# Performance work log

Measured on AMD Instinct MI355X. Metric: run time of the kernel, lower is better.

The kernel has to match this reference:

```python
import jax, jax.numpy as jnp
from jax import lax
import numpy as np

DECAY = 0.9
THRESH = 1.0


def setup_inputs() -> dict:
    key = jax.random.key(0)
    k1, k2, k3 = jax.random.split(key, 3)
    B, T, I, H, O = 64, 256, 1024, 2048, 1024
    x = jax.random.normal(k1, (B, T, I), dtype=jnp.float32)
    W1 = jax.random.normal(k2, (I, H), dtype=jnp.float32) * (1.0 / np.sqrt(I))
    b1 = jnp.zeros((H,), dtype=jnp.float32)
    W2 = jax.random.normal(k3, (H, O), dtype=jnp.float32) * (1.0 / np.sqrt(H))
    b2 = jnp.zeros((O,), dtype=jnp.float32)
    return {"x": x, "W1": W1, "b1": b1, "W2": W2, "b2": b2}


def reference(x, W1, b1, W2, b2):
    B, T, I = x.shape
    H = W1.shape[1]
    # Batch fc1 across all timesteps in one GEMM: [B,T,H]
    cur = jnp.einsum('bti,ih->bth', x, W1) + b1
    cur_tm = jnp.swapaxes(cur, 0, 1)  # [T,B,H] time-major for scan

    def step(carry, cur_t):
        mem, _ = carry
        mem = mem * DECAY + cur_t * (1.0 - DECAY)
        fired = mem > THRESH
        spk = jnp.where(fired, 1.0, 0.0).astype(mem.dtype)
        mem = jnp.where(fired, 0.0, mem)
        return (mem, spk), None

    mem0 = jnp.zeros((B, H), dtype=x.dtype)
    spk0 = jnp.zeros((B, H), dtype=x.dtype)
    (_, spk_last), _ = lax.scan(step, (mem0, spk0), cur_tm)
    # fc2 applied only to the final spike pattern, as in the original
    return spk_last @ W2 + b2
```

## Files before the change

### kernel.cpp

```cpp
#include <hip/hip_runtime.h>


typedef __attribute__((ext_vector_type(4))) float f32x4;
typedef __attribute__((ext_vector_type(8))) short s16x8;

#define GPTR(p) ((const __attribute__((address_space(1))) void*)(p))
#define SPTR(p) ((__attribute__((address_space(3))) void*)(p))

static constexpr int Bsz = 64, Tsz = 256, Isz = 1024, Hsz = 2048, Osz = 1024;
static constexpr int KB = 32;
static constexpr int NB = 64;

__device__ __forceinline__ unsigned short f2bf(float f) {
  unsigned u = __float_as_uint(f);
  u += 0x7FFFu + ((u >> 16) & 1u);
  return (unsigned short)(u >> 16);
}
__device__ __forceinline__ float bf2f(unsigned short h) {
  return __uint_as_float(((unsigned)h) << 16);
}

__global__ void split_x_kernel(const float* __restrict__ x,
                               unsigned short* __restrict__ hi,
                               unsigned short* __restrict__ lo) {
  const long i = (long)blockIdx.x * 256 + threadIdx.x;
  const float4 v = ((const float4*)x)[i];
  const unsigned short hx = f2bf(v.x), hy = f2bf(v.y), hz = f2bf(v.z), hw = f2bf(v.w);
  ushort4 H, L;
  H.x = hx; H.y = hy; H.z = hz; H.w = hw;
  L.x = f2bf(v.x - bf2f(hx));
  L.y = f2bf(v.y - bf2f(hy));
  L.z = f2bf(v.z - bf2f(hz));
  L.w = f2bf(v.w - bf2f(hw));
  ((ushort4*)hi)[i] = H;
  ((ushort4*)lo)[i] = L;
}

__global__ void w1_transpose_split_kernel(const float* __restrict__ W1,
                                          unsigned short* __restrict__ wh,
                                          unsigned short* __restrict__ wl) {
  __shared__ float tile[32][33];
  const int h0 = blockIdx.x * 32;
  const int i0 = blockIdx.y * 32;
  const int c = threadIdx.x & 31;
  const int r4 = threadIdx.x >> 5;
#pragma unroll
  for (int s = 0; s < 4; ++s) {
    const int r = r4 + s * 8;
    tile[r][c] = W1[(long)(i0 + r) * Hsz + h0 + c];
  }
  __syncthreads();
#pragma unroll
  for (int s = 0; s < 4; ++s) {
    const int hr = r4 + s * 8;
    const float v = tile[c][hr];
    const unsigned short hh = f2bf(v);
    wh[(long)(h0 + hr) * Isz + i0 + c] = hh;
    wl[(long)(h0 + hr) * Isz + i0 + c] = f2bf(v - bf2f(hh));
  }
}

__global__ __launch_bounds__(256, 3) void gemm1_scan_kernel(
    const unsigned short* __restrict__ xh, const unsigned short* __restrict__ xl,
    const unsigned short* __restrict__ wth, const unsigned short* __restrict__ wtl,
    const float* __restrict__ b1, float* __restrict__ spk) {
  __shared__ __align__(16) unsigned short lds[2 * Tsz * KB + 2 * NB * KB];
  unsigned short* ldsAh = lds;
  unsigned short* ldsAl = lds + Tsz * KB;
  unsigned short* ldsBh = lds + 2 * Tsz * KB;
  unsigned short* ldsBl = lds + 2 * Tsz * KB + NB * KB;

  const int tid = threadIdx.x;
  const int w = tid >> 6;
  const int l = tid & 63;
  const int b = blockIdx.y;
  const int hblk = blockIdx.x * NB;

  const int lr = l >> 2;
  const int lc = (l & 3) * 8;

  f32x4 acc[4][4];
#pragma unroll
  for (int i = 0; i < 4; ++i)
#pragma unroll
    for (int j = 0; j < 4; ++j)
      acc[i][j] = f32x4{0.f, 0.f, 0.f, 0.f};

  const long rowA0 = (long)b * Tsz;

  for (int kb = 0; kb < Isz / KB; ++kb) {
    const int k0 = kb * KB;
#pragma unroll
    for (int c = 0; c < 4; ++c) {
      const int rloc = w * 64 + c * 16;
      const unsigned short* gh = xh + (rowA0 + rloc + lr) * Isz + k0 + lc;
      const unsigned short* gl = xl + (rowA0 + rloc + lr) * Isz + k0 + lc;
      __builtin_amdgcn_global_load_lds(GPTR(gh), SPTR(ldsAh + rloc * KB), 16, 0, 0);
      __builtin_amdgcn_global_load_lds(GPTR(gl), SPTR(ldsAl + rloc * KB), 16, 0, 0);
    }
    {
      const int hloc = w * 16;
      const unsigned short* gh = wth + (long)(hblk + hloc + lr) * Isz + k0 + lc;
      const unsigned short* gl = wtl + (long)(hblk + hloc + lr) * Isz + k0 + lc;
      __builtin_amdgcn_global_load_lds(GPTR(gh), SPTR(ldsBh + hloc * KB), 16, 0, 0);
      __builtin_amdgcn_global_load_lds(GPTR(gl), SPTR(ldsBl + hloc * KB), 16, 0, 0);
    }
    __syncthreads();

    s16x8 ah[4], al[4];
    const int arow = w * 64 + (l & 15);
    const int koff = (l >> 4) * 8;
#pragma unroll
    for (int mi = 0; mi < 4; ++mi) {
      const int off = (arow + mi * 16) * KB + koff;
      ah[mi] = *(const s16x8*)(ldsAh + off);
      al[mi] = *(const s16x8*)(ldsAl + off);
    }
#pragma unroll
    for (int ni = 0; ni < 4; ++ni) {
      const int boff = (ni * 16 + (l & 15)) * KB + koff;
      const s16x8 bh = *(const s16x8*)(ldsBh + boff);
      const s16x8 bl = *(const s16x8*)(ldsBl + boff);
#pragma unroll
      for (int mi = 0; mi < 4; ++mi) {
        acc[mi][ni] = __builtin_amdgcn_mfma_f32_16x16x32_bf16(ah[mi], bh, acc[mi][ni], 0, 0, 0);
        acc[mi][ni] = __builtin_amdgcn_mfma_f32_16x16x32_bf16(ah[mi], bl, acc[mi][ni], 0, 0, 0);
        acc[mi][ni] = __builtin_amdgcn_mfma_f32_16x16x32_bf16(al[mi], bh, acc[mi][ni], 0, 0, 0);
      }
    }
    __syncthreads();
  }

  float* scanbuf = (float*)lds;
  float memv = 0.f;
  int fired = 0;
  const float b1v = (tid < NB) ? b1[hblk + tid] : 0.f;

  for (int p = 0; p < 4; ++p) {
    if (w == p) {
#pragma unroll
      for (int mi = 0; mi < 4; ++mi)
#pragma unroll
        for (int ni = 0; ni < 4; ++ni) {
          const int col = ni * 16 + (l & 15);
          const int trow = mi * 16 + (l >> 4) * 4;
#pragma unroll
          for (int r = 0; r < 4; ++r)
            scanbuf[(trow + r) * NB + col] = acc[mi][ni][r];
        }
    }
    __syncthreads();
    if (tid < NB) {
      for (int t = 0; t < 64; ++t) {
        const float c = scanbuf[t * NB + tid] + b1v;
        memv = memv * 0.9f + c * 0.1f;
        fired = memv > 1.0f;
        if (fired) memv = 0.f;
      }
    }
    __syncthreads();
  }
  if (tid < NB) spk[(long)b * Hsz + hblk + tid] = fired ? 1.0f : 0.0f;
}

__global__ void gemm2_kernel(const float* __restrict__ spk, const float* __restrict__ W2,
                             const float* __restrict__ b2, float* __restrict__ out) {
  __shared__ int s_cnt[256];
  __shared__ int s_off[257];
  __shared__ int s_list[Hsz];
  const int b = blockIdx.x;
  const int tid = threadIdx.x;
  int hs[8];
  int c = 0;
#pragma unroll
  for (int e = 0; e < 8; ++e) {
    const int h = tid * 8 + e;
    if (spk[(long)b * Hsz + h] > 0.5f) hs[c++] = h;
  }
  s_cnt[tid] = c;
  __syncthreads();
  if (tid == 0) {
    int s = 0;
    for (int i = 0; i < 256; ++i) { s_off[i] = s; s += s_cnt[i]; }
    s_off[256] = s;
  }
  __syncthreads();
  {
    const int base = s_off[tid];
    for (int i = 0; i < c; ++i) s_list[base + i] = hs[i];
  }
  __syncthreads();
  const int total = s_off[256];
#pragma unroll
  for (int q = 0; q < 4; ++q) {
    const int o = q * 256 + tid;
    float v = b2[o];
    for (int i = 0; i < total; ++i) v += W2[(long)s_list[i] * Osz + o];
    out[(long)b * Osz + o] = v;
  }
}

extern "C" void kernel_launch(void* const* d_in, const int* in_sizes, int n_in,
                              void* d_out, int out_size, void* d_ws, size_t ws_size,
                              hipStream_t stream) {
  const float* x  = (const float*)d_in[0];
  const float* W1 = (const float*)d_in[1];
  const float* b1 = (const float*)d_in[2];
  const float* W2 = (const float*)d_in[3];
  const float* b2 = (const float*)d_in[4];
  float* out = (float*)d_out;

  unsigned short* xh = (unsigned short*)d_ws;
  unsigned short* xl = xh + (long)Bsz * Tsz * Isz;
  unsigned short* wh = xl + (long)Bsz * Tsz * Isz;
  unsigned short* wl = wh + (long)Hsz * Isz;
  float* spk = (float*)(wl + (long)Hsz * Isz);

  split_x_kernel<<<(Bsz * Tsz * Isz) / (256 * 4), 256, 0, stream>>>(x, xh, xl);
  w1_transpose_split_kernel<<<dim3(Hsz / 32, Isz / 32), 256, 0, stream>>>(W1, wh, wl);
  gemm1_scan_kernel<<<dim3(Hsz / NB, Bsz), 256, 0, stream>>>(xh, xl, wh, wl, b1, spk);
  gemm2_kernel<<<Bsz, 256, 0, stream>>>(spk, W2, b2, out);
}
```

Baseline: 231.4 us.

## Restructure GEMM1 with 256x128 tiles, triple-buffered LDS pipeline and swizzle

The fused GEMM1+scan kernel moves from a 256x64 tile with 256 threads and single-buffered LDS to a 256x128 tile with 512 threads (8 waves in a 4x2 grid). Global-to-LDS loads are triple-buffered and interleaved in four phases with the MFMA work, using explicit waitcnt, barriers and s_setprio. The LDS layout is XOR-swizzled to reduce bank conflicts, and the block index is remapped so neighbouring blocks share data in cache. It also pads the scan buffer stride. The aim is to hide global load latency and raise MFMA utilisation, at the cost of more LDS per block (~120KB) and lower occupancy.

```diff
diff --git a/kernel.cpp b/kernel.cpp
--- a/kernel.cpp
+++ b/kernel.cpp
@@ -8,8 +8,12 @@
 #define SPTR(p) ((__attribute__((address_space(3))) void*)(p))
 
 static constexpr int Bsz = 64, Tsz = 256, Isz = 1024, Hsz = 2048, Osz = 1024;
-static constexpr int KB = 32;
-static constexpr int NB = 64;
+static constexpr int BM = 256, BN = 128, BK = 32;
+static constexpr int NKT = Isz / BK;
+static constexpr int AHALF = (BM / 2) * BK;
+static constexpr int ABUF = BM * BK;
+static constexpr int BBUF = BN * BK;
+static constexpr int BUFSZ = 2 * ABUF + 2 * BBUF;
 
 __device__ __forceinline__ unsigned short f2bf(float f) {
   unsigned u = __float_as_uint(f);
@@ -60,99 +64,157 @@
   }
 }
 
-__global__ __launch_bounds__(256, 3) void gemm1_scan_kernel(
+__global__ __launch_bounds__(512, 2) void gemm1_scan_kernel(
     const unsigned short* __restrict__ xh, const unsigned short* __restrict__ xl,
     const unsigned short* __restrict__ wth, const unsigned short* __restrict__ wtl,
     const float* __restrict__ b1, float* __restrict__ spk) {
-  __shared__ __align__(16) unsigned short lds[2 * Tsz * KB + 2 * NB * KB];
-  unsigned short* ldsAh = lds;
-  unsigned short* ldsAl = lds + Tsz * KB;
-  unsigned short* ldsBh = lds + 2 * Tsz * KB;
-  unsigned short* ldsBl = lds + 2 * Tsz * KB + NB * KB;
+  __shared__ __align__(16) unsigned short lds[3 * BUFSZ];
 
   const int tid = threadIdx.x;
+  const int l = tid & 63;
   const int w = tid >> 6;
-  const int l = tid & 63;
-  const int b = blockIdx.y;
-  const int hblk = blockIdx.x * NB;
-
-  const int lr = l >> 2;
-  const int lc = (l & 3) * 8;
+  const int wm = w >> 1;
+  const int wn = w & 1;
+
+  const int orig = blockIdx.y * 16 + blockIdx.x;
+  const int nid = (orig & 7) * 128 + (orig >> 3);
+  const int b = nid >> 4;
+  const int hblk = (nid & 15) * BN;
+
+  const int srow = tid >> 2;
+  const int gch = (tid & 3) ^ ((tid >> 3) & 3);
+  const unsigned short* gAh0 = xh + ((long)(b * Tsz) + srow) * Isz + gch * 8;
+  const unsigned short* gAh1 = xh + ((long)(b * Tsz) + 128 + srow) * Isz + gch * 8;
+  const unsigned short* gAl0 = xl + ((long)(b * Tsz) + srow) * Isz + gch * 8;
+  const unsigned short* gAl1 = xl + ((long)(b * Tsz) + 128 + srow) * Isz + gch * 8;
+  const unsigned short* gBh = wth + ((long)(hblk + srow)) * Isz + gch * 8;
+  const unsigned short* gBl = wtl + ((long)(hblk + srow)) * Isz + gch * 8;
+  const int ldst = tid * 8;
+
+#define ST_AH(Q, KT) do { unsigned short* d_ = lds + (Q) * BUFSZ + ldst;                        \
+    __builtin_amdgcn_global_load_lds(GPTR(gAh0 + (KT) * BK), SPTR(d_), 16, 0, 0);               \
+    __builtin_amdgcn_global_load_lds(GPTR(gAh1 + (KT) * BK), SPTR(d_ + AHALF), 16, 0, 0); } while (0)
+#define ST_AL(Q, KT) do { unsigned short* d_ = lds + (Q) * BUFSZ + ABUF + ldst;                 \
+    __builtin_amdgcn_global_load_lds(GPTR(gAl0 + (KT) * BK), SPTR(d_), 16, 0, 0);               \
+    __builtin_amdgcn_global_load_lds(GPTR(gAl1 + (KT) * BK), SPTR(d_ + AHALF), 16, 0, 0); } while (0)
+#define ST_BH(Q, KT) do { unsigned short* d_ = lds + (Q) * BUFSZ + 2 * ABUF + ldst;             \
+    __builtin_amdgcn_global_load_lds(GPTR(gBh + (KT) * BK), SPTR(d_), 16, 0, 0); } while (0)
+#define ST_BL(Q, KT) do { unsigned short* d_ = lds + (Q) * BUFSZ + 2 * ABUF + BBUF + ldst;      \
+    __builtin_amdgcn_global_load_lds(GPTR(gBl + (KT) * BK), SPTR(d_), 16, 0, 0); } while (0)
+
+  const int swz = ((l >> 4) ^ ((l >> 1) & 3)) * 8;
+  const int aBase = (wm * 64 + (l & 15)) * BK + swz;
+  const int bBase = (wn * 64 + (l & 15)) * BK + swz;
 
   f32x4 acc[4][4];
 #pragma unroll
   for (int i = 0; i < 4; ++i)
 #pragma unroll
-    for (int j = 0; j < 4; ++j)
-      acc[i][j] = f32x4{0.f, 0.f, 0.f, 0.f};
-
-  const long rowA0 = (long)b * Tsz;
-
-  for (int kb = 0; kb < Isz / KB; ++kb) {
-    const int k0 = kb * KB;
-#pragma unroll
-    for (int c = 0; c < 4; ++c) {
-      const int rloc = w * 64 + c * 16;
-      const unsigned short* gh = xh + (rowA0 + rloc + lr) * Isz + k0 + lc;
-      const unsigned short* gl = xl + (rowA0 + rloc + lr) * Isz + k0 + lc;
-      __builtin_amdgcn_global_load_lds(GPTR(gh), SPTR(ldsAh + rloc * KB), 16, 0, 0);
-      __builtin_amdgcn_global_load_lds(GPTR(gl), SPTR(ldsAl + rloc * KB), 16, 0, 0);
-    }
-    {
-      const int hloc = w * 16;
-      const unsigned short* gh = wth + (long)(hblk + hloc + lr) * Isz + k0 + lc;
-      const unsigned short* gl = wtl + (long)(hblk + hloc + lr) * Isz + k0 + lc;
-      __builtin_amdgcn_global_load_lds(GPTR(gh), SPTR(ldsBh + hloc * KB), 16, 0, 0);
-      __builtin_amdgcn_global_load_lds(GPTR(gl), SPTR(ldsBl + hloc * KB), 16, 0, 0);
-    }
-    __syncthreads();
-
-    s16x8 ah[4], al[4];
-    const int arow = w * 64 + (l & 15);
-    const int koff = (l >> 4) * 8;
-#pragma unroll
-    for (int mi = 0; mi < 4; ++mi) {
-      const int off = (arow + mi * 16) * KB + koff;
-      ah[mi] = *(const s16x8*)(ldsAh + off);
-      al[mi] = *(const s16x8*)(ldsAl + off);
-    }
-#pragma unroll
-    for (int ni = 0; ni < 4; ++ni) {
-      const int boff = (ni * 16 + (l & 15)) * KB + koff;
-      const s16x8 bh = *(const s16x8*)(ldsBh + boff);
-      const s16x8 bl = *(const s16x8*)(ldsBl + boff);
-#pragma unroll
-      for (int mi = 0; mi < 4; ++mi) {
-        acc[mi][ni] = __builtin_amdgcn_mfma_f32_16x16x32_bf16(ah[mi], bh, acc[mi][ni], 0, 0, 0);
-        acc[mi][ni] = __builtin_amdgcn_mfma_f32_16x16x32_bf16(ah[mi], bl, acc[mi][ni], 0, 0, 0);
-        acc[mi][ni] = __builtin_amdgcn_mfma_f32_16x16x32_bf16(al[mi], bh, acc[mi][ni], 0, 0, 0);
-      }
-    }
-    __syncthreads();
-  }
-
-  float* scanbuf = (float*)lds;
+    for (int j = 0; j < 4; ++j) acc[i][j] = f32x4{0.f, 0.f, 0.f, 0.f};
+
+  s16x8 Ah[4], Al[4], Bh[4], Bl[4];
+
+#define MM(MI, NI) do {                                                                          \
+    acc[MI][NI] = __builtin_amdgcn_mfma_f32_16x16x32_bf16(Ah[MI], Bh[NI], acc[MI][NI], 0, 0, 0); \
+    acc[MI][NI] = __builtin_amdgcn_mfma_f32_16x16x32_bf16(Ah[MI], Bl[NI], acc[MI][NI], 0, 0, 0); \
+    acc[MI][NI] = __builtin_amdgcn_mfma_f32_16x16x32_bf16(Al[MI], Bh[NI], acc[MI][NI], 0, 0, 0); \
+  } while (0)
+
+#define BAR() __builtin_amdgcn_s_barrier()
+#define LGKM0() do { asm volatile("s_waitcnt lgkmcnt(0)" ::: "memory");                          \
+    __builtin_amdgcn_sched_barrier(0); } while (0)
+
+  ST_AH(0, 0); ST_AL(0, 0); ST_BH(0, 0); ST_BL(0, 0);
+  ST_AH(1, 1); ST_AL(1, 1); ST_BH(1, 1); ST_BL(1, 1);
+  asm volatile("s_waitcnt vmcnt(6)" ::: "memory");
+  BAR();
+
+  int q = 0;
+  for (int kt = 0; kt < NKT; ++kt) {
+    const unsigned short* pAh = lds + q * BUFSZ;
+    const unsigned short* pAl = pAh + ABUF;
+    const unsigned short* pBh = pAh + 2 * ABUF;
+    const unsigned short* pBl = pBh + BBUF;
+    const int qn = (q >= 1) ? q - 1 : 2;
+    const bool st = (kt + 2) < NKT;
+    const int kst = kt + 2;
+
+    Ah[0] = *(const s16x8*)(pAh + aBase);
+    Al[0] = *(const s16x8*)(pAl + aBase);
+    Ah[1] = *(const s16x8*)(pAh + aBase + 512);
+    Al[1] = *(const s16x8*)(pAl + aBase + 512);
+    Bh[0] = *(const s16x8*)(pBh + bBase);
+    Bl[0] = *(const s16x8*)(pBl + bBase);
+    Bh[1] = *(const s16x8*)(pBh + bBase + 512);
+    Bl[1] = *(const s16x8*)(pBl + bBase + 512);
+    if (st) ST_AH(qn, kst);
+    BAR();
+    LGKM0();
+    __builtin_amdgcn_s_setprio(1);
+    MM(0, 0); MM(0, 1); MM(1, 0); MM(1, 1);
+    __builtin_amdgcn_s_setprio(0);
+    BAR();
+
+    Bh[2] = *(const s16x8*)(pBh + bBase + 1024);
+    Bl[2] = *(const s16x8*)(pBl + bBase + 1024);
+    Bh[3] = *(const s16x8*)(pBh + bBase + 1536);
+    Bl[3] = *(const s16x8*)(pBl + bBase + 1536);
+    if (st) ST_AL(qn, kst);
+    BAR();
+    LGKM0();
+    __builtin_amdgcn_s_setprio(1);
+    MM(0, 2); MM(0, 3); MM(1, 2); MM(1, 3);
+    __builtin_amdgcn_s_setprio(0);
+    BAR();
+
+    Ah[2] = *(const s16x8*)(pAh + aBase + 1024);
+    Al[2] = *(const s16x8*)(pAl + aBase + 1024);
+    Ah[3] = *(const s16x8*)(pAh + aBase + 1536);
+    Al[3] = *(const s16x8*)(pAl + aBase + 1536);
+    if (st) ST_BH(qn, kst);
+    BAR();
+    LGKM0();
+    __builtin_amdgcn_s_setprio(1);
+    MM(2, 0); MM(2, 1); MM(3, 0); MM(3, 1);
+    __builtin_amdgcn_s_setprio(0);
+    BAR();
+
+    if (st) ST_BL(qn, kst);
+    BAR();
+    LGKM0();
+    __builtin_amdgcn_s_setprio(1);
+    MM(2, 2); MM(2, 3); MM(3, 2); MM(3, 3);
+    __builtin_amdgcn_s_setprio(0);
+    if (kt < NKT - 2) asm volatile("s_waitcnt vmcnt(6)" ::: "memory");
+    else              asm volatile("s_waitcnt vmcnt(0)" ::: "memory");
+    BAR();
+
+    q = (q == 2) ? 0 : q + 1;
+  }
+
+  __syncthreads();
+  float* scanbuf = reinterpret_cast<float*>(lds);
   float memv = 0.f;
   int fired = 0;
-  const float b1v = (tid < NB) ? b1[hblk + tid] : 0.f;
+  const float b1v = b1[hblk + ((tid < BN) ? tid : 0)];
 
   for (int p = 0; p < 4; ++p) {
-    if (w == p) {
+    if (wm == p) {
 #pragma unroll
       for (int mi = 0; mi < 4; ++mi)
 #pragma unroll
         for (int ni = 0; ni < 4; ++ni) {
-          const int col = ni * 16 + (l & 15);
+          const int col = wn * 64 + ni * 16 + (l & 15);
           const int trow = mi * 16 + (l >> 4) * 4;
 #pragma unroll
           for (int r = 0; r < 4; ++r)
-            scanbuf[(trow + r) * NB + col] = acc[mi][ni][r];
+            scanbuf[(trow + r) * 132 + col] = acc[mi][ni][r];
         }
     }
     __syncthreads();
-    if (tid < NB) {
+    if (tid < BN) {
       for (int t = 0; t < 64; ++t) {
-        const float c = scanbuf[t * NB + tid] + b1v;
+        const float c = scanbuf[t * 132 + tid] + b1v;
         memv = memv * 0.9f + c * 0.1f;
         fired = memv > 1.0f;
         if (fired) memv = 0.f;
@@ -160,7 +222,7 @@
     }
     __syncthreads();
   }
-  if (tid < NB) spk[(long)b * Hsz + hblk + tid] = fired ? 1.0f : 0.0f;
+  if (tid < BN) spk[(long)b * Hsz + hblk + tid] = fired ? 1.0f : 0.0f;
 }
 
 __global__ void gemm2_kernel(const float* __restrict__ spk, const float* __restrict__ W2,
@@ -203,7 +265,7 @@
 extern "C" void kernel_launch(void* const* d_in, const int* in_sizes, int n_in,
                               void* d_out, int out_size, void* d_ws, size_t ws_size,
                               hipStream_t stream) {
-  const float* x  = (const float*)d_in[0];
+  const float* x = (const float*)d_in[0];
   const float* W1 = (const float*)d_in[1];
   const float* b1 = (const float*)d_in[2];
   const float* W2 = (const float*)d_in[3];
@@ -218,6 +280,6 @@
 
   split_x_kernel<<<(Bsz * Tsz * Isz) / (256 * 4), 256, 0, stream>>>(x, xh, xl);
   w1_transpose_split_kernel<<<dim3(Hsz / 32, Isz / 32), 256, 0, stream>>>(W1, wh, wl);
-  gemm1_scan_kernel<<<dim3(Hsz / NB, Bsz), 256, 0, stream>>>(xh, xl, wh, wl, b1, spk);
+  gemm1_scan_kernel<<<dim3(16, 64), 512, 0, stream>>>(xh, xl, wh, wl, b1, spk);
   gemm2_kernel<<<Bsz, 256, 0, stream>>>(spk, W2, b2, out);
 }
```

Result: no change. 229.1 us (-1.0%).

## Rewrite GEMM1 with 256x256 tiles, 32x32 MFMA, double-buffered swizzled LDS pipeline

Applied to the files above, without the earlier changes.

Reworks the fused GEMM1+scan kernel to use 512-thread blocks covering 256 hidden units, 32x32x16 bf16 MFMAs, XOR-swizzled LDS layout and a double-buffered, phase-staged global-to-LDS prefetch interleaved with compute via explicit waitcnt and barriers plus setprio. The goal is more data reuse per LDS byte, fewer bank conflicts, and overlap of memory loads with MFMA work instead of the previous load-sync-compute loop. It risks higher register pressure and reduced occupancy, and the hand-written vmcnt accounting must match the load ordering exactly. The scan phase is adapted to 256 columns over two 128-timestep rounds.

```diff
diff --git a/kernel.cpp b/kernel.cpp
--- a/kernel.cpp
+++ b/kernel.cpp
@@ -1,15 +1,17 @@
 #include <hip/hip_runtime.h>
 
 
-typedef __attribute__((ext_vector_type(4))) float f32x4;
+typedef __attribute__((ext_vector_type(16))) float f32x16;
 typedef __attribute__((ext_vector_type(8))) short s16x8;
 
 #define GPTR(p) ((const __attribute__((address_space(1))) void*)(p))
 #define SPTR(p) ((__attribute__((address_space(3))) void*)(p))
 
 static constexpr int Bsz = 64, Tsz = 256, Isz = 1024, Hsz = 2048, Osz = 1024;
-static constexpr int KB = 32;
-static constexpr int NB = 64;
+static constexpr int BK = 32;
+static constexpr int NKT = Isz / BK;
+static constexpr int AH_OFF = 0, AL_OFF = 8192, BH_OFF = 16384, BL_OFF = 24576;
+static constexpr int BUFEL = 32768;
 
 __device__ __forceinline__ unsigned short f2bf(float f) {
   unsigned u = __float_as_uint(f);
@@ -60,99 +62,174 @@
   }
 }
 
-__global__ __launch_bounds__(256, 3) void gemm1_scan_kernel(
+__global__ __launch_bounds__(512, 2) void gemm1_scan_kernel(
     const unsigned short* __restrict__ xh, const unsigned short* __restrict__ xl,
     const unsigned short* __restrict__ wth, const unsigned short* __restrict__ wtl,
     const float* __restrict__ b1, float* __restrict__ spk) {
-  __shared__ __align__(16) unsigned short lds[2 * Tsz * KB + 2 * NB * KB];
-  unsigned short* ldsAh = lds;
-  unsigned short* ldsAl = lds + Tsz * KB;
-  unsigned short* ldsBh = lds + 2 * Tsz * KB;
-  unsigned short* ldsBl = lds + 2 * Tsz * KB + NB * KB;
+  __shared__ __align__(16) unsigned short lds[2 * BUFEL];
 
   const int tid = threadIdx.x;
+  const int l = tid & 63;
   const int w = tid >> 6;
-  const int l = tid & 63;
+  const int wm = w >> 2;
+  const int wn = w & 3;
   const int b = blockIdx.y;
-  const int hblk = blockIdx.x * NB;
-
-  const int lr = l >> 2;
-  const int lc = (l & 3) * 8;
-
-  f32x4 acc[4][4];
+  const int hb = blockIdx.x * 256;
+
+  const int srow = tid >> 2;
+  const int gch8 = ((tid & 3) ^ ((tid >> 3) & 3)) * 8;
+  const long aoff0 = (long)(b * Tsz + srow) * Isz + gch8;
+  const long aoff1 = (long)(b * Tsz + 128 + srow) * Isz + gch8;
+  const long boff0 = (long)(hb + srow) * Isz + gch8;
+  const long boff1 = (long)(hb + 128 + srow) * Isz + gch8;
+  const unsigned short* gAh0 = xh + aoff0;  const unsigned short* gAh1 = xh + aoff1;
+  const unsigned short* gAl0 = xl + aoff0;  const unsigned short* gAl1 = xl + aoff1;
+  const unsigned short* gBh0 = wth + boff0; const unsigned short* gBh1 = wth + boff1;
+  const unsigned short* gBl0 = wtl + boff0; const unsigned short* gBl1 = wtl + boff1;
+
+#define STG(OFF, G0, G1, KT) do {                                                      \
+    unsigned short* d_ = lds + ((KT) & 1) * BUFEL + (OFF) + tid * 8;                   \
+    __builtin_amdgcn_global_load_lds(GPTR((G0) + (long)(KT) * BK), SPTR(d_), 16, 0, 0);\
+    __builtin_amdgcn_global_load_lds(GPTR((G1) + (long)(KT) * BK), SPTR(d_ + 4096), 16, 0, 0); \
+  } while (0)
+
+  const int lr = l & 31;
+  const int swzf = (l >> 1) & 3;
+  const int chK0 = (((l >> 5)) ^ swzf) * 8;
+  const int chK1 = ((2 + (l >> 5)) ^ swzf) * 8;
+  const int abase = (wm * 128 + lr) * 32;
+  const int bbase = (wn * 64 + lr) * 32;
+
+  f32x16 acc[4][2];
 #pragma unroll
   for (int i = 0; i < 4; ++i)
 #pragma unroll
-    for (int j = 0; j < 4; ++j)
-      acc[i][j] = f32x4{0.f, 0.f, 0.f, 0.f};
-
-  const long rowA0 = (long)b * Tsz;
-
-  for (int kb = 0; kb < Isz / KB; ++kb) {
-    const int k0 = kb * KB;
-#pragma unroll
-    for (int c = 0; c < 4; ++c) {
-      const int rloc = w * 64 + c * 16;
-      const unsigned short* gh = xh + (rowA0 + rloc + lr) * Isz + k0 + lc;
-      const unsigned short* gl = xl + (rowA0 + rloc + lr) * Isz + k0 + lc;
-      __builtin_amdgcn_global_load_lds(GPTR(gh), SPTR(ldsAh + rloc * KB), 16, 0, 0);
-      __builtin_amdgcn_global_load_lds(GPTR(gl), SPTR(ldsAl + rloc * KB), 16, 0, 0);
-    }
-    {
-      const int hloc = w * 16;
-      const unsigned short* gh = wth + (long)(hblk + hloc + lr) * Isz + k0 + lc;
-      const unsigned short* gl = wtl + (long)(hblk + hloc + lr) * Isz + k0 + lc;
-      __builtin_amdgcn_global_load_lds(GPTR(gh), SPTR(ldsBh + hloc * KB), 16, 0, 0);
-      __builtin_amdgcn_global_load_lds(GPTR(gl), SPTR(ldsBl + hloc * KB), 16, 0, 0);
-    }
-    __syncthreads();
-
-    s16x8 ah[4], al[4];
-    const int arow = w * 64 + (l & 15);
-    const int koff = (l >> 4) * 8;
+    for (int j = 0; j < 2; ++j) acc[i][j] = (f32x16)(0.f);
+
+#define MM(MI, NI, AF, BF) \
+  acc[MI][NI] = __builtin_amdgcn_mfma_f32_32x32x16_bf16(AF, BF, acc[MI][NI], 0, 0, 0)
+
+#define BAR() __builtin_amdgcn_s_barrier()
+#define LGKM0() do { asm volatile("s_waitcnt lgkmcnt(0)" ::: "memory");                \
+    __builtin_amdgcn_sched_barrier(0); } while (0)
+
+  STG(AH_OFF, gAh0, gAh1, 0);
+  STG(BH_OFF, gBh0, gBh1, 0);
+  STG(BL_OFF, gBl0, gBl1, 0);
+  STG(AL_OFF, gAl0, gAl1, 0);
+  asm volatile("s_waitcnt vmcnt(0)" ::: "memory");
+  BAR();
+
+  s16x8 Ah0[4], Ah1[4], Al0[4], Al1[4], Bh0[2], Bh1[2], Bl0[2], Bl1[2];
+
+  for (int kt = 0; kt < NKT; ++kt) {
+    const unsigned short* p = lds + (kt & 1) * BUFEL;
+    const bool st = (kt + 1) < NKT;
+
+#pragma unroll
+    for (int mi = 0; mi < 4; ++mi)
+      Ah0[mi] = *(const s16x8*)(p + AH_OFF + abase + mi * 1024 + chK0);
+#pragma unroll
+    for (int ni = 0; ni < 2; ++ni) {
+      Bh0[ni] = *(const s16x8*)(p + BH_OFF + bbase + ni * 1024 + chK0);
+      Bh1[ni] = *(const s16x8*)(p + BH_OFF + bbase + ni * 1024 + chK1);
+    }
+    if (st) STG(AH_OFF, gAh0, gAh1, kt + 1);
+    BAR();
+    LGKM0();
+    __builtin_amdgcn_s_setprio(1);
+    MM(0, 0, Ah0[0], Bh0[0]); MM(0, 1, Ah0[0], Bh0[1]);
+    MM(1, 0, Ah0[1], Bh0[0]); MM(1, 1, Ah0[1], Bh0[1]);
+    MM(2, 0, Ah0[2], Bh0[0]); MM(2, 1, Ah0[2], Bh0[1]);
+    MM(3, 0, Ah0[3], Bh0[0]); MM(3, 1, Ah0[3], Bh0[1]);
+    __builtin_amdgcn_s_setprio(0);
+    if (st) asm volatile("s_waitcnt vmcnt(4)" ::: "memory");
+    else    asm volatile("s_waitcnt vmcnt(2)" ::: "memory");
+    BAR();
+
+#pragma unroll
+    for (int mi = 0; mi < 4; ++mi)
+      Ah1[mi] = *(const s16x8*)(p + AH_OFF + abase + mi * 1024 + chK1);
+#pragma unroll
+    for (int ni = 0; ni < 2; ++ni) {
+      Bl0[ni] = *(const s16x8*)(p + BL_OFF + bbase + ni * 1024 + chK0);
+      Bl1[ni] = *(const s16x8*)(p + BL_OFF + bbase + ni * 1024 + chK1);
+    }
+    if (st) STG(BH_OFF, gBh0, gBh1, kt + 1);
+    BAR();
+    LGKM0();
+    __builtin_amdgcn_s_setprio(1);
+    MM(0, 0, Ah1[0], Bh1[0]); MM(0, 1, Ah1[0], Bh1[1]);
+    MM(1, 0, Ah1[1], Bh1[0]); MM(1, 1, Ah1[1], Bh1[1]);
+    MM(2, 0, Ah1[2], Bh1[0]); MM(2, 1, Ah1[2], Bh1[1]);
+    MM(3, 0, Ah1[3], Bh1[0]); MM(3, 1, Ah1[3], Bh1[1]);
+    __builtin_amdgcn_s_setprio(0);
+    if (st) asm volatile("s_waitcnt vmcnt(4)" ::: "memory");
+    else    asm volatile("s_waitcnt vmcnt(0)" ::: "memory");
+    BAR();
+
+    if (st) STG(BL_OFF, gBl0, gBl1, kt + 1);
+    BAR();
+    LGKM0();
+    __builtin_amdgcn_s_setprio(1);
+    MM(0, 0, Ah0[0], Bl0[0]); MM(0, 1, Ah0[0], Bl0[1]);
+    MM(1, 0, Ah0[1], Bl0[0]); MM(1, 1, Ah0[1], Bl0[1]);
+    MM(2, 0, Ah0[2], Bl0[0]); MM(2, 1, Ah0[2], Bl0[1]);
+    MM(3, 0, Ah0[3], Bl0[0]); MM(3, 1, Ah0[3], Bl0[1]);
+    MM(0, 0, Ah1[0], Bl1[0]); MM(0, 1, Ah1[0], Bl1[1]);
+    MM(1, 0, Ah1[1], Bl1[0]); MM(1, 1, Ah1[1], Bl1[1]);
+    MM(2, 0, Ah1[2], Bl1[0]); MM(2, 1, Ah1[2], Bl1[1]);
+    MM(3, 0, Ah1[3], Bl1[0]); MM(3, 1, Ah1[3], Bl1[1]);
+    __builtin_amdgcn_s_setprio(0);
+    if (st) asm volatile("s_waitcnt vmcnt(4)" ::: "memory");
+    BAR();
+
 #pragma unroll
     for (int mi = 0; mi < 4; ++mi) {
-      const int off = (arow + mi * 16) * KB + koff;
-      ah[mi] = *(const s16x8*)(ldsAh + off);
-      al[mi] = *(const s16x8*)(ldsAl + off);
-    }
-#pragma unroll
-    for (int ni = 0; ni < 4; ++ni) {
-      const int boff = (ni * 16 + (l & 15)) * KB + koff;
-      const s16x8 bh = *(const s16x8*)(ldsBh + boff);
-      const s16x8 bl = *(const s16x8*)(ldsBl + boff);
-#pragma unroll
-      for (int mi = 0; mi < 4; ++mi) {
-        acc[mi][ni] = __builtin_amdgcn_mfma_f32_16x16x32_bf16(ah[mi], bh, acc[mi][ni], 0, 0, 0);
-        acc[mi][ni] = __builtin_amdgcn_mfma_f32_16x16x32_bf16(ah[mi], bl, acc[mi][ni], 0, 0, 0);
-        acc[mi][ni] = __builtin_amdgcn_mfma_f32_16x16x32_bf16(al[mi], bh, acc[mi][ni], 0, 0, 0);
-      }
-    }
-    __syncthreads();
-  }
-
-  float* scanbuf = (float*)lds;
+      Al0[mi] = *(const s16x8*)(p + AL_OFF + abase + mi * 1024 + chK0);
+      Al1[mi] = *(const s16x8*)(p + AL_OFF + abase + mi * 1024 + chK1);
+    }
+    if (st) STG(AL_OFF, gAl0, gAl1, kt + 1);
+    BAR();
+    LGKM0();
+    __builtin_amdgcn_s_setprio(1);
+    MM(0, 0, Al0[0], Bh0[0]); MM(0, 1, Al0[0], Bh0[1]);
+    MM(1, 0, Al0[1], Bh0[0]); MM(1, 1, Al0[1], Bh0[1]);
+    MM(2, 0, Al0[2], Bh0[0]); MM(2, 1, Al0[2], Bh0[1]);
+    MM(3, 0, Al0[3], Bh0[0]); MM(3, 1, Al0[3], Bh0[1]);
+    MM(0, 0, Al1[0], Bh1[0]); MM(0, 1, Al1[0], Bh1[1]);
+    MM(1, 0, Al1[1], Bh1[0]); MM(1, 1, Al1[1], Bh1[1]);
+    MM(2, 0, Al1[2], Bh1[0]); MM(2, 1, Al1[2], Bh1[1]);
+    MM(3, 0, Al1[3], Bh1[0]); MM(3, 1, Al1[3], Bh1[1]);
+    __builtin_amdgcn_s_setprio(0);
+    if (st) asm volatile("s_waitcnt vmcnt(4)" ::: "memory");
+    BAR();
+  }
+
+  __syncthreads();
+  float* scanbuf = reinterpret_cast<float*>(lds);
   float memv = 0.f;
   int fired = 0;
-  const float b1v = (tid < NB) ? b1[hblk + tid] : 0.f;
-
-  for (int p = 0; p < 4; ++p) {
-    if (w == p) {
+  const float b1v = b1[hb + ((tid < 256) ? tid : 0)];
+
+  for (int rnd = 0; rnd < 2; ++rnd) {
+    if (wm == rnd) {
 #pragma unroll
       for (int mi = 0; mi < 4; ++mi)
 #pragma unroll
-        for (int ni = 0; ni < 4; ++ni) {
-          const int col = ni * 16 + (l & 15);
-          const int trow = mi * 16 + (l >> 4) * 4;
-#pragma unroll
-          for (int r = 0; r < 4; ++r)
-            scanbuf[(trow + r) * NB + col] = acc[mi][ni][r];
+        for (int ni = 0; ni < 2; ++ni) {
+          const int col = wn * 64 + ni * 32 + lr;
+#pragma unroll
+          for (int r = 0; r < 16; ++r) {
+            const int trow = mi * 32 + (r & 3) + 8 * (r >> 2) + 4 * (l >> 5);
+            scanbuf[trow * 256 + col] = acc[mi][ni][r];
+          }
         }
     }
     __syncthreads();
-    if (tid < NB) {
-      for (int t = 0; t < 64; ++t) {
-        const float c = scanbuf[t * NB + tid] + b1v;
+    if (tid < 256) {
+      for (int t = 0; t < 128; ++t) {
+        const float c = scanbuf[t * 256 + tid] + b1v;
         memv = memv * 0.9f + c * 0.1f;
         fired = memv > 1.0f;
         if (fired) memv = 0.f;
@@ -160,7 +237,7 @@
     }
     __syncthreads();
   }
-  if (tid < NB) spk[(long)b * Hsz + hblk + tid] = fired ? 1.0f : 0.0f;
+  if (tid < 256) spk[(long)b * Hsz + hb + tid] = fired ? 1.0f : 0.0f;
 }
 
 __global__ void gemm2_kernel(const float* __restrict__ spk, const float* __restrict__ W2,
@@ -203,7 +280,7 @@
 extern "C" void kernel_launch(void* const* d_in, const int* in_sizes, int n_in,
                               void* d_out, int out_size, void* d_ws, size_t ws_size,
                               hipStream_t stream) {
-  const float* x  = (const float*)d_in[0];
+  const float* x = (const float*)d_in[0];
   const float* W1 = (const float*)d_in[1];
   const float* b1 = (const float*)d_in[2];
   const float* W2 = (const float*)d_in[3];
@@ -218,6 +295,6 @@
 
   split_x_kernel<<<(Bsz * Tsz * Isz) / (256 * 4), 256, 0, stream>>>(x, xh, xl);
   w1_transpose_split_kernel<<<dim3(Hsz / 32, Isz / 32), 256, 0, stream>>>(W1, wh, wl);
-  gemm1_scan_kernel<<<dim3(Hsz / NB, Bsz), 256, 0, stream>>>(xh, xl, wh, wl, b1, spk);
+  gemm1_scan_kernel<<<dim3(8, 64), 512, 0, stream>>>(xh, xl, wh, wl, b1, spk);
   gemm2_kernel<<<Bsz, 256, 0, stream>>>(spk, W2, b2, out);
 }
```

New measurement: 208.8 us. -9.8%, faster.
